# Performance work log

Measured on AMD Instinct MI355X. Metric: run time of the kernel, lower is better.

The kernel has to match this reference:

```python
import jax, jax.numpy as jnp
import numpy as np

C = 256
C8 = C // 8


def setup_inputs() -> dict:
    key = jax.random.key(0)
    ks = jax.random.split(key, 9)
    B, H, W = 4, 64, 64
    inp = jax.random.normal(ks[0], (B, C, H, W), dtype=jnp.float32)
    original = jax.random.normal(ks[1], (B, C, H, W), dtype=jnp.float32)
    s = 1.0 / np.sqrt(C)
    wq = jax.random.normal(ks[2], (C8, C), dtype=jnp.float32) * s
    bq = jax.random.normal(ks[3], (C8,), dtype=jnp.float32) * 0.01
    wk = jax.random.normal(ks[4], (C8, C), dtype=jnp.float32) * s
    bk = jax.random.normal(ks[5], (C8,), dtype=jnp.float32) * 0.01
    wv = jax.random.normal(ks[6], (C, C), dtype=jnp.float32) * s
    bv = jax.random.normal(ks[7], (C,), dtype=jnp.float32) * 0.01
    # torch inits gamma to 0; use a nonzero value so the attention branch contributes
    gamma = jnp.asarray([0.5], dtype=jnp.float32)
    return {"input": inp, "original": original, "wq": wq, "bq": bq,
            "wk": wk, "bk": bk, "wv": wv, "bv": bv, "gamma": gamma}


def reference(input, original, wq, bq, wk, bk, wv, bv, gamma):
    B, Cc, H, W = input.shape
    HW = H * W
    x = input.reshape(B, Cc, HW)          # [B, C, HW]
    o = original.reshape(B, Cc, HW)
    # 1x1 convs == per-pixel linear projections
    q = jnp.einsum('oc,bcn->bno', wq, x) + bq          # [B, HW, C8]
    k = jnp.einsum('oc,bcn->bon', wk, x) + bk[:, None]  # [B, C8, HW]
    v = jnp.einsum('oc,bcn->bon', wv, o) + bv[:, None]  # [B, C, HW]
    attn = jax.nn.softmax(jnp.einsum('bic,bcj->bij', q, k), axis=-1)  # [B, HW, HW]
    out = jnp.einsum('bcj,bij->bci', v, attn)           # [B, C, HW]
    out = out.reshape(B, Cc, H, W)
    return gamma[0] * out + input
```

## Files before the change

kernel.cpp:

```cpp
#include <hip/hip_runtime.h>

typedef short s16x8 __attribute__((ext_vector_type(8)));
typedef float f32x4 __attribute__((ext_vector_type(4)));
typedef float f32x16 __attribute__((ext_vector_type(16)));

#define B_ 4
#define C_ 256
#define S_ 4096
#define LOG2E 1.44269504088896f
#define M2 32.0f

#if __has_builtin(__builtin_amdgcn_exp2f)
#define EXP2(x) __builtin_amdgcn_exp2f(x)
#else
#define EXP2(x) __exp2f(x)
#endif

__device__ __forceinline__ unsigned short f2b(float f) {
  union { float f; unsigned u; } v; v.f = f;
  unsigned r = v.u + 0x7fffu + ((v.u >> 16) & 1u);
  return (unsigned short)(r >> 16);
}
__device__ __forceinline__ unsigned short f2b_fast(float f) {
  union { float f; unsigned u; } v; v.f = f;
  return (unsigned short)((v.u + 0x8000u) >> 16);
}
__device__ __forceinline__ s16x8 lds_ld8(const unsigned short* p) {
  union { s16x8 v; uint2 u[2]; } r;
  r.u[0] = *(const uint2*)p;
  r.u[1] = *(const uint2*)(p + 4);
  return r.v;
}

__global__ __launch_bounds__(256)
void prep_kernel(const float* __restrict__ wq, const float* __restrict__ wk,
                 const float* __restrict__ wv,
                 unsigned short* __restrict__ Wvf, unsigned short* __restrict__ Wqkf) {
  const int G = (blockIdx.x * 256 + threadIdx.x) * 4;
  union { unsigned short us[4]; uint2 u2; } pk;
  if (G < 65536) {
    const int e0 = G & 7, lane = (G >> 3) & 63, ks16 = (G >> 9) & 15;
    const int mt = (G >> 13) & 1, cg = G >> 14;
    const int row = cg * 64 + mt * 32 + (lane & 31);
    const int k   = ks16 * 16 + (lane >> 5) * 8 + e0;
    f32x4 v = *(const f32x4*)(wv + (size_t)row * 256 + k);
    #pragma unroll
    for (int i = 0; i < 4; ++i) pk.us[i] = f2b(v[i]);
    *(uint2*)(Wvf + G) = pk.u2;
  } else {
    const int H = G - 65536;
    const int e0 = H & 7, lane = (H >> 3) & 63, ks16 = (H >> 9) & 15;
    const int mt = (H >> 13) & 1;
    const int row = lane & 31;
    const int k   = ks16 * 16 + (lane >> 5) * 8 + e0;
    const float* src = mt ? wk : wq;
    f32x4 v = *(const f32x4*)(src + (size_t)row * 256 + k);
    if (mt == 0) v = v * LOG2E;
    #pragma unroll
    for (int i = 0; i < 4; ++i) pk.us[i] = f2b(v[i]);
    *(uint2*)(Wqkf + H) = pk.u2;
  }
}

__global__ __launch_bounds__(256, 2)
void qkproj_kernel(const float* __restrict__ x,
                   const float* __restrict__ bq, const float* __restrict__ bk,
                   const unsigned short* __restrict__ Wqkf,
                   unsigned short* __restrict__ Qb, unsigned short* __restrict__ Kb) {
  __shared__ union {
    unsigned short Sl[64 * 260];
    unsigned short Rl[64 * 68];
  } um;
  const int jt = blockIdx.x, b = blockIdx.y;
  const int n0 = jt * 64;
  const int t = threadIdx.x;
  const int L = t & 63, w = t >> 6;
  const int g = L >> 5, l32 = L & 31;
  const float* xb = x + (size_t)b * C_ * S_;
  #pragma unroll
  for (int hp = 0; hp < 2; ++hp) {
    const int c8 = hp * 128 + (t >> 4) * 8;
    const int n4 = (t & 15) * 4;
    f32x4 v[8];
    #pragma unroll
    for (int j = 0; j < 8; ++j)
      v[j] = *(const f32x4*)(xb + (size_t)(c8 + j) * S_ + n0 + n4);
    #pragma unroll
    for (int k = 0; k < 4; ++k) {
      union { unsigned short us[8]; uint2 u2[2]; } pk;
      #pragma unroll
      for (int j = 0; j < 8; ++j) pk.us[j] = f2b(v[j][k]);
      *(uint2*)&um.Sl[(n4 + k) * 260 + c8]     = pk.u2[0];
      *(uint2*)&um.Sl[(n4 + k) * 260 + c8 + 4] = pk.u2[1];
    }
  }
  __syncthreads();
  const int mt = w >> 1, nt = w & 1;
  f32x16 acc = (f32x16)0.0f;
  #pragma unroll
  for (int ks = 0; ks < 16; ++ks) {
    s16x8 af = *(const s16x8*)(Wqkf + ((size_t)(mt * 16 + ks) * 64 + L) * 8);
    s16x8 bf = lds_ld8(&um.Sl[(nt * 32 + l32) * 260 + ks * 16 + g * 8]);
    acc = __builtin_amdgcn_mfma_f32_32x32x16_bf16(af, bf, acc, 0, 0, 0);
  }
  __syncthreads();
  const int n = nt * 32 + l32;
  #pragma unroll
  for (int reg = 0; reg < 16; ++reg) {
    const int rr = (reg & 3) + 8 * (reg >> 2) + 4 * g;
    const float val = (mt == 0) ? acc[reg] + bq[rr] * LOG2E : acc[reg] + bk[rr];
    um.Rl[n * 68 + mt * 32 + rr] = f2b(val);
  }
  __syncthreads();
  const int nn = t >> 2, ch0 = (t & 3) * 16;
  s16x8 a = lds_ld8(um.Rl + nn * 68 + ch0);
  s16x8 cvec = lds_ld8(um.Rl + nn * 68 + ch0 + 8);
  unsigned short* dst = (ch0 < 32)
      ? Qb + ((size_t)b * S_ + n0 + nn) * 32 + ch0
      : Kb + ((size_t)b * S_ + n0 + nn) * 32 + (ch0 - 32);
  *(s16x8*)dst = a;
  *(s16x8*)(dst + 8) = cvec;
}

__global__ __launch_bounds__(512, 2)
void vproj_kernel(const float* __restrict__ orig, const float* __restrict__ bv,
                  const unsigned short* __restrict__ Wvf,
                  unsigned short* __restrict__ Vf) {
  __shared__ union {
    unsigned short Sl[64 * 260];
    unsigned short Rv[256 * 68];
  } um;
  const int jt = blockIdx.x, b = blockIdx.y;
  const int n0 = jt * 64;
  const int t = threadIdx.x;
  const int L = t & 63, w = t >> 6;
  const int g = L >> 5, l32 = L & 31;
  const float* ob = orig + (size_t)b * C_ * S_;
  {
    const int c8 = (t >> 4) * 8;
    const int n4 = (t & 15) * 4;
    f32x4 v[8];
    #pragma unroll
    for (int j = 0; j < 8; ++j)
      v[j] = *(const f32x4*)(ob + (size_t)(c8 + j) * S_ + n0 + n4);
    #pragma unroll
    for (int k = 0; k < 4; ++k) {
      union { unsigned short us[8]; uint2 u2[2]; } pk;
      #pragma unroll
      for (int j = 0; j < 8; ++j) pk.us[j] = f2b(v[j][k]);
      *(uint2*)&um.Sl[(n4 + k) * 260 + c8]     = pk.u2[0];
      *(uint2*)&um.Sl[(n4 + k) * 260 + c8 + 4] = pk.u2[1];
    }
  }
  __syncthreads();
  f32x16 acc0 = (f32x16)0.0f, acc1 = (f32x16)0.0f;
  #pragma unroll
  for (int ks = 0; ks < 16; ++ks) {
    s16x8 af  = *(const s16x8*)(Wvf + ((size_t)(w * 16 + ks) * 64 + L) * 8);
    s16x8 bf0 = lds_ld8(&um.Sl[l32 * 260 + ks * 16 + g * 8]);
    s16x8 bf1 = lds_ld8(&um.Sl[(32 + l32) * 260 + ks * 16 + g * 8]);
    acc0 = __builtin_amdgcn_mfma_f32_32x32x16_bf16(af, bf0, acc0, 0, 0, 0);
    acc1 = __builtin_amdgcn_mfma_f32_32x32x16_bf16(af, bf1, acc1, 0, 0, 0);
  }
  __syncthreads();
  const int pi0 = (l32 & 15) * 4 + (l32 >> 4);
  #pragma unroll
  for (int reg = 0; reg < 16; ++reg) {
    const int rr = (reg & 3) + 8 * (reg >> 2) + 4 * g;
    const int ch = w * 32 + rr;
    const float bias = bv[ch];
    um.Rv[ch * 68 + pi0]     = f2b(acc0[reg] + bias);
    um.Rv[ch * 68 + pi0 + 2] = f2b(acc1[reg] + bias);
  }
  __syncthreads();
  unsigned short* Vtile = Vf + (size_t)(b * 64 + jt) * 4 * 4096;
  #pragma unroll
  for (int k = 0; k < 4; ++k) {
    const int cI = k * 512 + t;
    const int cgc = cI >> 9, r = cI & 511;
    const int vv = r >> 8, kb = (r >> 6) & 3, Lf = r & 63;
    const int chl = cgc * 64 + vv * 32 + (Lf & 31);
    const int jj  = kb * 16 + (Lf >> 5) * 8;
    s16x8 vvv = lds_ld8(&um.Rv[chl * 68 + jj]);
    *(s16x8*)(Vtile + (size_t)cI * 8) = vvv;
  }
}

struct FlashSmem {
  union {
    unsigned short P[2][64 * 132];
    float scr[2][32 * 258];
  } u;
  float lpart[2][64];
  float invl[64];
};

__global__ __launch_bounds__(512, 2)
void flash_kernel(const unsigned short* __restrict__ Qb,
                  const unsigned short* __restrict__ Kb,
                  const unsigned short* __restrict__ Vf,
                  const float* __restrict__ inp,
                  const float* __restrict__ gamma,
                  float* __restrict__ out) {
  __shared__ FlashSmem sm;
  const int l  = blockIdx.x;
  const int b  = (l & 7) >> 1;
  const int i0 = ((l >> 3) * 2 + (l & 1)) * 64;
  const int t  = threadIdx.x;
  const int L = t & 63, w = t >> 6;
  const int q4 = L >> 4, c16 = L & 15;
  const int g  = L >> 5, l32 = L & 31;
  const int rh = w & 3, jh = w >> 2;
  const int cg = w & 3, dup = w >> 2;
  const float gam = gamma[0];
  const unsigned short* Kbb = Kb + (size_t)b * S_ * 32;
  const unsigned short* Vbb = Vf + (size_t)b * 64 * 4 * 4096;
  const s16x8 qf = *(const s16x8*)(Qb + ((size_t)b * S_ + i0 + rh * 16 + c16) * 32 + q4 * 8);

  f32x16 acc00 = (f32x16)0.0f, acc01 = (f32x16)0.0f;
  f32x16 acc10 = (f32x16)0.0f, acc11 = (f32x16)0.0f;
  float lp[4] = {0.f, 0.f, 0.f, 0.f};

  s16x8 kc[4], kn[4];
  #pragma unroll
  for (int tt = 0; tt < 2; ++tt) {
    kc[tt * 2 + 0] = *(const s16x8*)(Kbb + (size_t)(tt * 64 + jh * 32 + c16) * 32 + q4 * 8);
    kc[tt * 2 + 1] = *(const s16x8*)(Kbb + (size_t)(tt * 64 + jh * 32 + 16 + c16) * 32 + q4 * 8);
  }

  for (int c = 0; c < 32; ++c) {
    s16x8 vf0[4], vf1[4];
    if (c > 0) {
      const unsigned short* vb = Vbb + (size_t)(((c - 1) * 2 + dup) * 4 + cg) * 4096;
      #pragma unroll
      for (int kb = 0; kb < 4; ++kb) {
        vf0[kb] = *(const s16x8*)(vb + kb * 512 + L * 8);
        vf1[kb] = *(const s16x8*)(vb + 2048 + kb * 512 + L * 8);
      }
    }
    if (c < 31) {
      const unsigned short* kbase = Kbb + (size_t)(c + 1) * 128 * 32;
      #pragma unroll
      for (int tt = 0; tt < 2; ++tt) {
        kn[tt * 2 + 0] = *(const s16x8*)(kbase + (size_t)(tt * 64 + jh * 32 + c16) * 32 + q4 * 8);
        kn[tt * 2 + 1] = *(const s16x8*)(kbase + (size_t)(tt * 64 + jh * 32 + 16 + c16) * 32 + q4 * 8);
      }
    }
    unsigned short* Pw = sm.u.P[c & 1];
    #pragma unroll
    for (int tt = 0; tt < 2; ++tt) {
      const f32x4 cinit = (f32x4)(-M2);
      f32x4 s0 = __builtin_amdgcn_mfma_f32_16x16x32_bf16(qf, kc[tt * 2 + 0], cinit, 0, 0, 0);
      f32x4 s1 = __builtin_amdgcn_mfma_f32_16x16x32_bf16(qf, kc[tt * 2 + 1], cinit, 0, 0, 0);
      #pragma unroll
      for (int r = 0; r < 4; ++r) {
        const float p0 = EXP2(s0[r]);
        const float p1 = EXP2(s1[r]);
        lp[r] += p0 + p1;
        const int row = rh * 16 + q4 * 4 + r;
        const unsigned pack = (unsigned)f2b_fast(p0) | ((unsigned)f2b_fast(p1) << 16);
        *(unsigned*)&Pw[row * 132 + tt * 64 + c16 * 4 + jh * 2] = pack;
      }
    }
    if (c > 0) {
      const unsigned short* Pr = sm.u.P[(c - 1) & 1];
      #pragma unroll
      for (int kb = 0; kb < 4; ++kb) {
        const int ko = dup * 64 + kb * 16 + g * 8;
        const s16x8 pf0 = lds_ld8(Pr + l32 * 132 + ko);
        const s16x8 pf1 = lds_ld8(Pr + (32 + l32) * 132 + ko);
        acc00 = __builtin_amdgcn_mfma_f32_32x32x16_bf16(pf0, vf0[kb], acc00, 0, 0, 0);
        acc01 = __builtin_amdgcn_mfma_f32_32x32x16_bf16(pf0, vf1[kb], acc01, 0, 0, 0);
        acc10 = __builtin_amdgcn_mfma_f32_32x32x16_bf16(pf1, vf0[kb], acc10, 0, 0, 0);
        acc11 = __builtin_amdgcn_mfma_f32_32x32x16_bf16(pf1, vf1[kb], acc11, 0, 0, 0);
      }
    }
    __syncthreads();
    #pragma unroll
    for (int i = 0; i < 4; ++i) kc[i] = kn[i];
  }
  {
    const unsigned short* vb = Vbb + (size_t)((62 + dup) * 4 + cg) * 4096;
    s16x8 vf0[4], vf1[4];
    #pragma unroll
    for (int kb = 0; kb < 4; ++kb) {
      vf0[kb] = *(const s16x8*)(vb + kb * 512 + L * 8);
      vf1[kb] = *(const s16x8*)(vb + 2048 + kb * 512 + L * 8);
    }
    const unsigned short* Pr = sm.u.P[1];
    #pragma unroll
    for (int kb = 0; kb < 4; ++kb) {
      const int ko = dup * 64 + kb * 16 + g * 8;
      const s16x8 pf0 = lds_ld8(Pr + l32 * 132 + ko);
      const s16x8 pf1 = lds_ld8(Pr + (32 + l32) * 132 + ko);
      acc00 = __builtin_amdgcn_mfma_f32_32x32x16_bf16(pf0, vf0[kb], acc00, 0, 0, 0);
      acc01 = __builtin_amdgcn_mfma_f32_32x32x16_bf16(pf0, vf1[kb], acc01, 0, 0, 0);
      acc10 = __builtin_amdgcn_mfma_f32_32x32x16_bf16(pf1, vf0[kb], acc10, 0, 0, 0);
      acc11 = __builtin_amdgcn_mfma_f32_32x32x16_bf16(pf1, vf1[kb], acc11, 0, 0, 0);
    }
  }
  #pragma unroll
  for (int r = 0; r < 4; ++r) {
    float v = lp[r];
    #pragma unroll
    for (int d = 1; d < 16; d <<= 1) v += __shfl_xor(v, d, 64);
    lp[r] = v;
  }
  if (c16 == 0) {
    #pragma unroll
    for (int r = 0; r < 4; ++r) sm.lpart[jh][rh * 16 + q4 * 4 + r] = lp[r];
  }
  __syncthreads();
  if (t < 64) sm.invl[t] = gam / (sm.lpart[0][t] + sm.lpart[1][t]);
  #pragma unroll
  for (int h = 0; h < 2; ++h) {
    const f32x16 a0 = h ? acc10 : acc00;
    const f32x16 a1 = h ? acc11 : acc01;
    float* pl = sm.u.scr[dup];
    #pragma unroll
    for (int reg = 0; reg < 16; ++reg) {
      const int rr = (reg & 3) + 8 * (reg >> 2) + 4 * g;
      pl[rr * 258 + cg * 64 + l32]      = a0[reg];
      pl[rr * 258 + cg * 64 + 32 + l32] = a1[reg];
    }
    __syncthreads();
    const int ch = t >> 1;
    const int il16 = (t & 1) * 16;
    #pragma unroll
    for (int q = 0; q < 4; ++q) {
      const int iloc = il16 + q * 4;
      const size_t gi = ((size_t)b * C_ + ch) * S_ + i0 + h * 32 + iloc;
      const f32x4 iv = *(const f32x4*)(inp + gi);
      f32x4 o;
      #pragma unroll
      for (int k = 0; k < 4; ++k) {
        const int il = iloc + k;
        o[k] = (sm.u.scr[0][il * 258 + ch] + sm.u.scr[1][il * 258 + ch]) * sm.invl[h * 32 + il] + iv[k];
      }
      *(f32x4*)(out + gi) = o;
    }
    __syncthreads();
  }
}

extern "C" void kernel_launch(void* const* d_in, const int* in_sizes, int n_in,
                              void* d_out, int out_size, void* d_ws, size_t ws_size,
                              hipStream_t stream) {
  const float* inp   = (const float*)d_in[0];
  const float* orig  = (const float*)d_in[1];
  const float* wq    = (const float*)d_in[2];
  const float* bq    = (const float*)d_in[3];
  const float* wk    = (const float*)d_in[4];
  const float* bk    = (const float*)d_in[5];
  const float* wv    = (const float*)d_in[6];
  const float* bv    = (const float*)d_in[7];
  const float* gamma = (const float*)d_in[8];
  float* out = (float*)d_out;

  unsigned short* Qb = (unsigned short*)d_ws;
  unsigned short* Kb = Qb + (size_t)B_ * S_ * 32;
  unsigned short* Vf = Kb + (size_t)B_ * S_ * 32;
  unsigned short* Wvf  = (unsigned short*)((char*)d_out + (size_t)out_size * 4 - 262144);
  unsigned short* Wqkf = Wvf + 65536;

  prep_kernel<<<80, 256, 0, stream>>>(wq, wk, wv, Wvf, Wqkf);
  qkproj_kernel<<<dim3(64, 4), 256, 0, stream>>>(inp, bq, bk, Wqkf, Qb, Kb);
  vproj_kernel<<<dim3(64, 4), 512, 0, stream>>>(orig, bv, Wvf, Vf);
  flash_kernel<<<256, 512, 0, stream>>>(Qb, Kb, Vf, inp, gamma, out);
}
```

Before: 172.6 us.

## Retile flash kernel to 128 query rows by 128 channels with LDS-staged K

The flash kernel now gives each block 128 query rows and half of the channels (128) instead of 64 rows and all 256 channels. Each wave computes the scores for a full 128-key chunk, so the two warp groups no longer each hold a partial row sum that must be merged. K chunks are staged through a double-buffered LDS tile rather than loaded into registers per wave, and the V projection writes a new layout matching 128-key, 128-channel chunks. The aim is to reuse each P tile over more channels per wave and simplify the epilogue. The cost is that QK^T and the exponentials are now computed twice, once per channel half, and the P buffer in LDS doubles in size, which may reduce occupancy.

```diff
diff --git a/kernel.cpp b/kernel.cpp
--- a/kernel.cpp
+++ b/kernel.cpp
@@ -163,36 +163,39 @@
     acc1 = __builtin_amdgcn_mfma_f32_32x32x16_bf16(af, bf1, acc1, 0, 0, 0);
   }
   __syncthreads();
-  const int pi0 = (l32 & 15) * 4 + (l32 >> 4);
+  const int chw = w * 32;
   #pragma unroll
   for (int reg = 0; reg < 16; ++reg) {
     const int rr = (reg & 3) + 8 * (reg >> 2) + 4 * g;
-    const int ch = w * 32 + rr;
-    const float bias = bv[ch];
-    um.Rv[ch * 68 + pi0]     = f2b(acc0[reg] + bias);
-    um.Rv[ch * 68 + pi0 + 2] = f2b(acc1[reg] + bias);
-  }
-  __syncthreads();
-  unsigned short* Vtile = Vf + (size_t)(b * 64 + jt) * 4 * 4096;
-  #pragma unroll
-  for (int k = 0; k < 4; ++k) {
-    const int cI = k * 512 + t;
-    const int cgc = cI >> 9, r = cI & 511;
-    const int vv = r >> 8, kb = (r >> 6) & 3, Lf = r & 63;
-    const int chl = cgc * 64 + vv * 32 + (Lf & 31);
-    const int jj  = kb * 16 + (Lf >> 5) * 8;
-    s16x8 vvv = lds_ld8(&um.Rv[chl * 68 + jj]);
-    *(s16x8*)(Vtile + (size_t)cI * 8) = vvv;
+    const float bias = bv[chw + rr];
+    um.Rv[(chw + rr) * 68 + l32]      = f2b(acc0[reg] + bias);
+    um.Rv[(chw + rr) * 68 + 32 + l32] = f2b(acc1[reg] + bias);
+  }
+  __syncthreads();
+  const int chunk = jt >> 1, par = jt & 1;
+  #pragma unroll
+  for (int k = 0; k < 8; ++k) {
+    const int id = k * 512 + t;
+    const int c16v = id >> 8;
+    const int ch = id & 255;
+    union { unsigned short us[4]; uint2 u2; } pk;
+    #pragma unroll
+    for (int u = 0; u < 4; ++u)
+      pk.us[u] = um.Rv[ch * 68 + u * 16 + c16v];
+    const int kb = c16v >> 1, g8 = c16v & 1;
+    const size_t base = ((size_t)((b * 32 + chunk) * 2 + (ch >> 7)) * 4 + ((ch >> 5) & 3)) * 4096;
+    *(uint2*)(Vf + base + kb * 512 + (g8 * 32 + (ch & 31)) * 8 + par * 4) = pk.u2;
   }
 }
 
 struct FlashSmem {
   union {
-    unsigned short P[2][64 * 132];
-    float scr[2][32 * 258];
+    unsigned short P[2][128 * 132];
+    float scr[32 * 130];
   } u;
-  float lpart[2][64];
-  float invl[64];
+  __align__(16) unsigned short Kl[2][128 * 40];
+  float lvec[128];
+  float invl[128];
 };
 
 __global__ __launch_bounds__(512, 2)
@@ -203,55 +206,47 @@
                   const float* __restrict__ gamma,
                   float* __restrict__ out) {
   __shared__ FlashSmem sm;
-  const int l  = blockIdx.x;
-  const int b  = (l & 7) >> 1;
-  const int i0 = ((l >> 3) * 2 + (l & 1)) * 64;
-  const int t  = threadIdx.x;
+  const int l   = blockIdx.x;
+  const int b   = (l & 7) >> 1;
+  const int chh = l & 1;
+  const int i0  = (l >> 3) * 128;
+  const int ch0 = chh * 128;
+  const int t = threadIdx.x;
   const int L = t & 63, w = t >> 6;
   const int q4 = L >> 4, c16 = L & 15;
   const int g  = L >> 5, l32 = L & 31;
-  const int rh = w & 3, jh = w >> 2;
-  const int cg = w & 3, dup = w >> 2;
+  const int rh = w;
+  const int cg = w & 3, ih = w >> 2;
   const float gam = gamma[0];
   const unsigned short* Kbb = Kb + (size_t)b * S_ * 32;
-  const unsigned short* Vbb = Vf + (size_t)b * 64 * 4 * 4096;
   const s16x8 qf = *(const s16x8*)(Qb + ((size_t)b * S_ + i0 + rh * 16 + c16) * 32 + q4 * 8);
 
-  f32x16 acc00 = (f32x16)0.0f, acc01 = (f32x16)0.0f;
-  f32x16 acc10 = (f32x16)0.0f, acc11 = (f32x16)0.0f;
+  f32x16 acc0 = (f32x16)0.0f, acc1 = (f32x16)0.0f;
   float lp[4] = {0.f, 0.f, 0.f, 0.f};
 
-  s16x8 kc[4], kn[4];
-  #pragma unroll
-  for (int tt = 0; tt < 2; ++tt) {
-    kc[tt * 2 + 0] = *(const s16x8*)(Kbb + (size_t)(tt * 64 + jh * 32 + c16) * 32 + q4 * 8);
-    kc[tt * 2 + 1] = *(const s16x8*)(Kbb + (size_t)(tt * 64 + jh * 32 + 16 + c16) * 32 + q4 * 8);
-  }
+  *(s16x8*)&sm.Kl[0][(t >> 2) * 40 + (t & 3) * 8] = *(const s16x8*)(Kbb + t * 8);
+  __syncthreads();
 
   for (int c = 0; c < 32; ++c) {
-    s16x8 vf0[4], vf1[4];
+    s16x8 vf[8];
     if (c > 0) {
-      const unsigned short* vb = Vbb + (size_t)(((c - 1) * 2 + dup) * 4 + cg) * 4096;
-      #pragma unroll
-      for (int kb = 0; kb < 4; ++kb) {
-        vf0[kb] = *(const s16x8*)(vb + kb * 512 + L * 8);
-        vf1[kb] = *(const s16x8*)(vb + 2048 + kb * 512 + L * 8);
-      }
-    }
-    if (c < 31) {
-      const unsigned short* kbase = Kbb + (size_t)(c + 1) * 128 * 32;
-      #pragma unroll
-      for (int tt = 0; tt < 2; ++tt) {
-        kn[tt * 2 + 0] = *(const s16x8*)(kbase + (size_t)(tt * 64 + jh * 32 + c16) * 32 + q4 * 8);
-        kn[tt * 2 + 1] = *(const s16x8*)(kbase + (size_t)(tt * 64 + jh * 32 + 16 + c16) * 32 + q4 * 8);
-      }
-    }
+      const unsigned short* vb = Vf + ((size_t)((b * 32 + (c - 1)) * 2 + chh) * 4 + cg) * 4096;
+      #pragma unroll
+      for (int kb = 0; kb < 8; ++kb)
+        vf[kb] = *(const s16x8*)(vb + kb * 512 + L * 8);
+    }
+    if (c < 31)
+      *(s16x8*)&sm.Kl[(c + 1) & 1][(t >> 2) * 40 + (t & 3) * 8] =
+          *(const s16x8*)(Kbb + (size_t)(c + 1) * 4096 + t * 8);
     unsigned short* Pw = sm.u.P[c & 1];
-    #pragma unroll
-    for (int tt = 0; tt < 2; ++tt) {
+    const unsigned short* Klc = sm.Kl[c & 1];
+    #pragma unroll
+    for (int u = 0; u < 4; ++u) {
+      const s16x8 kf0 = *(const s16x8*)(Klc + ((2 * u + 0) * 16 + c16) * 40 + q4 * 8);
+      const s16x8 kf1 = *(const s16x8*)(Klc + ((2 * u + 1) * 16 + c16) * 40 + q4 * 8);
       const f32x4 cinit = (f32x4)(-M2);
-      f32x4 s0 = __builtin_amdgcn_mfma_f32_16x16x32_bf16(qf, kc[tt * 2 + 0], cinit, 0, 0, 0);
-      f32x4 s1 = __builtin_amdgcn_mfma_f32_16x16x32_bf16(qf, kc[tt * 2 + 1], cinit, 0, 0, 0);
+      f32x4 s0 = __builtin_amdgcn_mfma_f32_16x16x32_bf16(qf, kf0, cinit, 0, 0, 0);
+      f32x4 s1 = __builtin_amdgcn_mfma_f32_16x16x32_bf16(qf, kf1, cinit, 0, 0, 0);
       #pragma unroll
       for (int r = 0; r < 4; ++r) {
         const float p0 = EXP2(s0[r]);
@@ -259,44 +254,36 @@
         lp[r] += p0 + p1;
         const int row = rh * 16 + q4 * 4 + r;
         const unsigned pack = (unsigned)f2b_fast(p0) | ((unsigned)f2b_fast(p1) << 16);
-        *(unsigned*)&Pw[row * 132 + tt * 64 + c16 * 4 + jh * 2] = pack;
+        *(unsigned*)&Pw[row * 132 + c16 * 8 + 2 * u] = pack;
       }
     }
     if (c > 0) {
       const unsigned short* Pr = sm.u.P[(c - 1) & 1];
       #pragma unroll
-      for (int kb = 0; kb < 4; ++kb) {
-        const int ko = dup * 64 + kb * 16 + g * 8;
-        const s16x8 pf0 = lds_ld8(Pr + l32 * 132 + ko);
-        const s16x8 pf1 = lds_ld8(Pr + (32 + l32) * 132 + ko);
-        acc00 = __builtin_amdgcn_mfma_f32_32x32x16_bf16(pf0, vf0[kb], acc00, 0, 0, 0);
-        acc01 = __builtin_amdgcn_mfma_f32_32x32x16_bf16(pf0, vf1[kb], acc01, 0, 0, 0);
-        acc10 = __builtin_amdgcn_mfma_f32_32x32x16_bf16(pf1, vf0[kb], acc10, 0, 0, 0);
-        acc11 = __builtin_amdgcn_mfma_f32_32x32x16_bf16(pf1, vf1[kb], acc11, 0, 0, 0);
+      for (int kb = 0; kb < 8; ++kb) {
+        const int ko = kb * 16 + g * 8;
+        const s16x8 pf0 = lds_ld8(Pr + (ih * 64 + l32) * 132 + ko);
+        const s16x8 pf1 = lds_ld8(Pr + (ih * 64 + 32 + l32) * 132 + ko);
+        acc0 = __builtin_amdgcn_mfma_f32_32x32x16_bf16(pf0, vf[kb], acc0, 0, 0, 0);
+        acc1 = __builtin_amdgcn_mfma_f32_32x32x16_bf16(pf1, vf[kb], acc1, 0, 0, 0);
       }
     }
     __syncthreads();
-    #pragma unroll
-    for (int i = 0; i < 4; ++i) kc[i] = kn[i];
   }
   {
-    const unsigned short* vb = Vbb + (size_t)((62 + dup) * 4 + cg) * 4096;
-    s16x8 vf0[4], vf1[4];
-    #pragma unroll
-    for (int kb = 0; kb < 4; ++kb) {
-      vf0[kb] = *(const s16x8*)(vb + kb * 512 + L * 8);
-      vf1[kb] = *(const s16x8*)(vb + 2048 + kb * 512 + L * 8);
-    }
+    const unsigned short* vb = Vf + ((size_t)((b * 32 + 31) * 2 + chh) * 4 + cg) * 4096;
+    s16x8 vf[8];
+    #pragma unroll
+    for (int kb = 0; kb < 8; ++kb)
+      vf[kb] = *(const s16x8*)(vb + kb * 512 + L * 8);
     const unsigned short* Pr = sm.u.P[1];
     #pragma unroll
-    for (int kb = 0; kb < 4; ++kb) {
-      const int ko = dup * 64 + kb * 16 + g * 8;
-      const s16x8 pf0 = lds_ld8(Pr + l32 * 132 + ko);
-      const s16x8 pf1 = lds_ld8(Pr + (32 + l32) * 132 + ko);
-      acc00 = __builtin_amdgcn_mfma_f32_32x32x16_bf16(pf0, vf0[kb], acc00, 0, 0, 0);
-      acc01 = __builtin_amdgcn_mfma_f32_32x32x16_bf16(pf0, vf1[kb], acc01, 0, 0, 0);
-      acc10 = __builtin_amdgcn_mfma_f32_32x32x16_bf16(pf1, vf0[kb], acc10, 0, 0, 0);
-      acc11 = __builtin_amdgcn_mfma_f32_32x32x16_bf16(pf1, vf1[kb], acc11, 0, 0, 0);
+    for (int kb = 0; kb < 8; ++kb) {
+      const int ko = kb * 16 + g * 8;
+      const s16x8 pf0 = lds_ld8(Pr + (ih * 64 + l32) * 132 + ko);
+      const s16x8 pf1 = lds_ld8(Pr + (ih * 64 + 32 + l32) * 132 + ko);
+      acc0 = __builtin_amdgcn_mfma_f32_32x32x16_bf16(pf0, vf[kb], acc0, 0, 0, 0);
+      acc1 = __builtin_amdgcn_mfma_f32_32x32x16_bf16(pf1, vf[kb], acc1, 0, 0, 0);
     }
   }
   #pragma unroll
@@ -308,37 +295,36 @@
   }
   if (c16 == 0) {
     #pragma unroll
-    for (int r = 0; r < 4; ++r) sm.lpart[jh][rh * 16 + q4 * 4 + r] = lp[r];
-  }
-  __syncthreads();
-  if (t < 64) sm.invl[t] = gam / (sm.lpart[0][t] + sm.lpart[1][t]);
-  #pragma unroll
-  for (int h = 0; h < 2; ++h) {
-    const f32x16 a0 = h ? acc10 : acc00;
-    const f32x16 a1 = h ? acc11 : acc01;
-    float* pl = sm.u.scr[dup];
-    #pragma unroll
-    for (int reg = 0; reg < 16; ++reg) {
-      const int rr = (reg & 3) + 8 * (reg >> 2) + 4 * g;
-      pl[rr * 258 + cg * 64 + l32]      = a0[reg];
-      pl[rr * 258 + cg * 64 + 32 + l32] = a1[reg];
+    for (int r = 0; r < 4; ++r) sm.lvec[rh * 16 + q4 * 4 + r] = lp[r];
+  }
+  __syncthreads();
+  if (t < 128) sm.invl[t] = gam / sm.lvec[t];
+  #pragma unroll
+  for (int h = 0; h < 4; ++h) {
+    if (ih == (h >> 1)) {
+      const f32x16 a = (h & 1) ? acc1 : acc0;
+      #pragma unroll
+      for (int reg = 0; reg < 16; ++reg) {
+        const int rr = (reg & 3) + 8 * (reg >> 2) + 4 * g;
+        sm.u.scr[rr * 130 + cg * 32 + l32] = a[reg];
+      }
     }
     __syncthreads();
-    const int ch = t >> 1;
-    const int il16 = (t & 1) * 16;
-    #pragma unroll
-    for (int q = 0; q < 4; ++q) {
-      const int iloc = il16 + q * 4;
-      const size_t gi = ((size_t)b * C_ + ch) * S_ + i0 + h * 32 + iloc;
-      const f32x4 iv = *(const f32x4*)(inp + gi);
-      f32x4 o;
-      #pragma unroll
-      for (int k = 0; k < 4; ++k) {
-        const int il = iloc + k;
-        o[k] = (sm.u.scr[0][il * 258 + ch] + sm.u.scr[1][il * 258 + ch]) * sm.invl[h * 32 + il] + iv[k];
-      }
-      *(f32x4*)(out + gi) = o;
-    }
+    const int ch = t >> 2;
+    const int i4 = (t & 3) * 8;
+    const f32x4 sc0 = *(const f32x4*)&sm.invl[h * 32 + i4];
+    const f32x4 sc1 = *(const f32x4*)&sm.invl[h * 32 + i4 + 4];
+    const size_t gi = ((size_t)(b * C_ + ch0 + ch)) * S_ + i0 + h * 32 + i4;
+    const f32x4 in0 = *(const f32x4*)(inp + gi);
+    const f32x4 in1 = *(const f32x4*)(inp + gi + 4);
+    f32x4 o0, o1;
+    #pragma unroll
+    for (int k = 0; k < 4; ++k) {
+      o0[k] = sm.u.scr[(i4 + k) * 130 + ch] * sc0[k] + in0[k];
+      o1[k] = sm.u.scr[(i4 + 4 + k) * 130 + ch] * sc1[k] + in1[k];
+    }
+    *(f32x4*)(out + gi)     = o0;
+    *(f32x4*)(out + gi + 4) = o1;
     __syncthreads();
   }
 }
```

Measured after the change: 184.3 us. 1.07x slower.
